# Kernel tuning notes

Measured on AMD Instinct MI355X. Metric: run time of the kernel, lower is better.

Reference implementation:

```python
import jax, jax.numpy as jnp
import numpy as np

NQ = 100000  # Query nodes
NP = 100000  # Product nodes
E = 600000   # edges per relation
D_IN = 128
D_H = 128
# relation r: (src_type, dst_type); 0=Query, 1=Product
# 0: Click Q->P, 1: reverse_Click P->Q, 2: reverse_QueryResult P->Q, 3: QueryResult Q->P
REL = [(0, 1), (1, 0), (1, 0), (0, 1)]
N_NODES = [NQ, NP]


def setup_inputs() -> dict:
    key = jax.random.key(0)
    ks = jax.random.split(key, 12)
    s = 1.0 / np.sqrt(D_IN)  # keep activations well-scaled across 2 layers
    return {
        "x_query": jax.random.normal(ks[0], (NQ, D_IN), jnp.float32),
        "x_product": jax.random.normal(ks[1], (NP, D_IN), jnp.float32),
        "src_idx": jax.random.randint(ks[2], (4, E), 0, NQ, jnp.int32),
        "dst_idx": jax.random.randint(ks[3], (4, E), 0, NP, jnp.int32),
        "W_self1": jax.random.normal(ks[4], (4, D_IN, D_H), jnp.float32) * s,
        "W_neigh1": jax.random.normal(ks[5], (4, D_IN, D_H), jnp.float32) * s,
        "b1": jnp.zeros((4, D_H), jnp.float32),
        "W_self2": jax.random.normal(ks[6], (4, D_H, D_H), jnp.float32) * s,
        "W_neigh2": jax.random.normal(ks[7], (4, D_H, D_H), jnp.float32) * s,
        "b2": jnp.zeros((4, D_H), jnp.float32),
    }


def _hetero_sage_layer(h, W_self, W_neigh, b, src_idx, dst_idx):
    # h: [h_query, h_product]; per-relation SAGEConv(mean), cross-relation sum
    acc = [None, None]
    for r, (s, t) in enumerate(REL):
        nt = N_NODES[t]
        msg = h[s][src_idx[r]]                                   # [E, d] gather
        neigh_sum = jax.ops.segment_sum(msg, dst_idx[r], num_segments=nt)
        deg = jax.ops.segment_sum(jnp.ones((E,), h[s].dtype), dst_idx[r],
                                  num_segments=nt)
        neigh_mean = neigh_sum / jnp.maximum(deg, 1.0)[:, None]
        out = h[t] @ W_self[r] + neigh_mean @ W_neigh[r] + b[r]
        acc[t] = out if acc[t] is None else acc[t] + out
    return acc


def reference(x_query, x_product, src_idx, dst_idx,
              W_self1, W_neigh1, b1, W_self2, W_neigh2, b2):
    h = [x_query, x_product]
    h = _hetero_sage_layer(h, W_self1, W_neigh1, b1, src_idx, dst_idx)
    h = [jax.nn.relu(v) for v in h]  # ReLU only between layers
    h = _hetero_sage_layer(h, W_self2, W_neigh2, b2, src_idx, dst_idx)
    return (h[0], h[1])  # (H_query, H_product)
```

## Files before the change

### kernel.cpp

```cpp
#include <hip/hip_runtime.h>
#include <hip/hip_bf16.h>

#define N_NODES 100000
#define NEDGE   600000
#define SCAN_B  1024
#define NBLK    98
#define BSHIFT  9
#define NBUCK   196
#define BCAP    3456

typedef __attribute__((ext_vector_type(8))) short bf16x8;
typedef __attribute__((ext_vector_type(4))) short s16x4;
typedef __attribute__((ext_vector_type(4))) float f32x4;
typedef __attribute__((ext_vector_type(4))) unsigned u32x4;
typedef __attribute__((ext_vector_type(2))) int int2v;

__device__ __forceinline__ short f2bf(float f) {
  union { float f; unsigned u; } x; x.f = f;
  unsigned r = x.u + 0x7FFFu + ((x.u >> 16) & 1u);
  return (short)(r >> 16);
}

__global__ __launch_bounds__(256) void bin_k(const int* __restrict__ sidx,
                                             const int* __restrict__ didx,
                                             int* __restrict__ bincnt,
                                             int2v* __restrict__ stage) {
  __shared__ int hist[NBUCK];
  __shared__ int base[NBUCK];
  int r = blockIdx.y, t = threadIdx.x;
  int e0 = blockIdx.x * 2048 + t;
  const int* dd = didx + (size_t)r * NEDGE;
  const int* ss = sidx + (size_t)r * NEDGE;
  for (int i = t; i < NBUCK; i += 256) hist[i] = 0;
  __syncthreads();
  int sv[8], dv[8], bu[8], lr[8];
#pragma unroll
  for (int j = 0; j < 8; ++j) {
    int e = e0 + j * 256;
    if (e < NEDGE) {
      dv[j] = dd[e]; sv[j] = ss[e];
      bu[j] = dv[j] >> BSHIFT;
      lr[j] = atomicAdd(&hist[bu[j]], 1);
    }
  }
  __syncthreads();
  for (int i = t; i < NBUCK; i += 256)
    base[i] = atomicAdd(&bincnt[r * NBUCK + i], hist[i]);
  __syncthreads();
#pragma unroll
  for (int j = 0; j < 8; ++j) {
    int e = e0 + j * 256;
    if (e < NEDGE)
      stage[(size_t)(r * NBUCK + bu[j]) * BCAP + base[bu[j]] + lr[j]] =
          (int2v){sv[j], dv[j]};
  }
}

__global__ __launch_bounds__(256) void hist_k(const int2v* __restrict__ stage,
                                              const int* __restrict__ bincnt,
                                              int* __restrict__ cnt) {
  __shared__ int h[512];
  int bu = blockIdx.x, r = blockIdx.y, t = threadIdx.x;
  int len = bincnt[r * NBUCK + bu];
  const int2v* sg = stage + (size_t)(r * NBUCK + bu) * BCAP;
  h[t] = 0; h[t + 256] = 0;
  __syncthreads();
  int lo = bu << BSHIFT;
  for (int i = t; i < len; i += 256) atomicAdd(&h[sg[i].y - lo], 1);
  __syncthreads();
  int d0 = lo + t;
  if (d0 < N_NODES)       cnt[r * N_NODES + d0]       = h[t];
  if (d0 + 256 < N_NODES) cnt[r * N_NODES + d0 + 256] = h[t + 256];
}

__global__ __launch_bounds__(256) void scan1_k(const int* __restrict__ cnt,
                                               int* __restrict__ bsum) {
  __shared__ int lds[256];
  int b = blockIdx.x, r = blockIdx.y, t = threadIdx.x;
  int i0 = b * SCAN_B + t * 4;
  int s = 0;
#pragma unroll
  for (int j = 0; j < 4; ++j)
    if (i0 + j < N_NODES) s += cnt[r * N_NODES + i0 + j];
  lds[t] = s;
  __syncthreads();
  for (int st = 128; st > 0; st >>= 1) {
    if (t < st) lds[t] += lds[t + st];
    __syncthreads();
  }
  if (t == 0) bsum[r * NBLK + b] = lds[0];
}

__global__ __launch_bounds__(128) void scan2_k(int* __restrict__ bsum) {
  __shared__ int buf[128];
  int t = threadIdx.x;
  for (int r = 0; r < 4; ++r) {
    int v = (t < NBLK) ? bsum[r * NBLK + t] : 0;
    buf[t] = v;
    __syncthreads();
    for (int st = 1; st < 128; st <<= 1) {
      int x = (t >= st) ? buf[t - st] : 0;
      __syncthreads();
      buf[t] += x;
      __syncthreads();
    }
    if (t < NBLK) bsum[r * NBLK + t] = buf[t] - v;
    __syncthreads();
  }
}

__global__ __launch_bounds__(256) void scan3_k(const int* __restrict__ cnt,
                                               const int* __restrict__ bsum,
                                               int* __restrict__ off) {
  __shared__ int lds[256];
  int b = blockIdx.x, r = blockIdx.y, t = threadIdx.x;
  int i0 = b * SCAN_B + t * 4;
  int c[4] = {0, 0, 0, 0};
#pragma unroll
  for (int j = 0; j < 4; ++j)
    if (i0 + j < N_NODES) c[j] = cnt[r * N_NODES + i0 + j];
  int s = c[0] + c[1] + c[2] + c[3];
  lds[t] = s;
  __syncthreads();
  for (int st = 1; st < 256; st <<= 1) {
    int x = (t >= st) ? lds[t - st] : 0;
    __syncthreads();
    lds[t] += x;
    __syncthreads();
  }
  int run = bsum[r * NBLK + b] + lds[t] - s;
  int* o = off + r * (N_NODES + 1);
#pragma unroll
  for (int j = 0; j < 4; ++j) {
    if (i0 + j < N_NODES) { o[i0 + j] = run; run += c[j]; }
  }
  if (b == 0 && t == 0) o[N_NODES] = NEDGE;
}

__global__ __launch_bounds__(256) void place_k(const int2v* __restrict__ stage,
                                               const int* __restrict__ bincnt,
                                               const int* __restrict__ off,
                                               int* __restrict__ csr) {
  __shared__ int ofl[512];
  __shared__ int cur[512];
  int bu = blockIdx.x, r = blockIdx.y, t = threadIdx.x;
  int len = bincnt[r * NBUCK + bu];
  const int2v* sg = stage + (size_t)(r * NBUCK + bu) * BCAP;
  const int* of = off + r * (N_NODES + 1);
  int* cs = csr + (size_t)r * NEDGE;
  int lo = bu << BSHIFT;
  int d0 = lo + t;
  ofl[t]       = (d0 < N_NODES) ? of[d0] : 0;
  ofl[t + 256] = (d0 + 256 < N_NODES) ? of[d0 + 256] : 0;
  cur[t] = 0; cur[t + 256] = 0;
  __syncthreads();
  for (int i = t; i < len; i += 256) {
    int2v sd = sg[i];
    int dl = sd.y - lo;
    int pos = ofl[dl] + atomicAdd(&cur[dl], 1);
    cs[pos] = sd.x;
  }
}

__global__ __launch_bounds__(256) void cvt2_k(const float* __restrict__ x0,
                                              const float* __restrict__ x1,
                                              unsigned* __restrict__ o0,
                                              unsigned* __restrict__ o1) {
  const float* x = blockIdx.y ? x1 : x0;
  unsigned* o = blockIdx.y ? o1 : o0;
  int i = blockIdx.x * 256 + threadIdx.x;
  if (i >= N_NODES * 16) return;
  f32x4 v0 = ((const f32x4*)x)[i * 2];
  f32x4 v1 = ((const f32x4*)x)[i * 2 + 1];
  unsigned r0 = (unsigned)(unsigned short)f2bf(v0[0]) |
                ((unsigned)(unsigned short)f2bf(v0[1]) << 16);
  unsigned r1 = (unsigned)(unsigned short)f2bf(v0[2]) |
                ((unsigned)(unsigned short)f2bf(v0[3]) << 16);
  unsigned r2 = (unsigned)(unsigned short)f2bf(v1[0]) |
                ((unsigned)(unsigned short)f2bf(v1[1]) << 16);
  unsigned r3 = (unsigned)(unsigned short)f2bf(v1[2]) |
                ((unsigned)(unsigned short)f2bf(v1[3]) << 16);
  ((u32x4*)o)[i] = (u32x4){r0, r1, r2, r3};
}

__global__ __launch_bounds__(256) void prep_w_k(const float* __restrict__ Ws1,
                                                const float* __restrict__ Wn1,
                                                const float* __restrict__ Ws2,
                                                const float* __restrict__ Wn2,
                                                short* __restrict__ WTp) {
  int tid = blockIdx.x * 256 + threadIdx.x;
  int lane = tid & 63;
  int n0 = (tid >> 6) & 7;
  int idx3 = tid >> 9;
  int k0 = idx3 % 12;
  int lt = idx3 / 12;
  int l = lt >> 1, t = lt & 1;
  const float* Wself  = l ? Ws2 : Ws1;
  const float* Wneigh = l ? Wn2 : Wn1;
  int rA = t ? 0 : 1, rB = t ? 3 : 2;
  int n = n0 * 16 + (lane & 15);
  int kbase = k0 * 32 + (lane >> 4) * 8;
  short out[8];
#pragma unroll
  for (int j = 0; j < 8; ++j) {
    int k = kbase + j;
    int kk = k & 127, blk = k >> 7;
    float v;
    if (blk == 0)      v = Wself[rA * 16384 + kk * 128 + n] + Wself[rB * 16384 + kk * 128 + n];
    else if (blk == 1) v = Wneigh[rA * 16384 + kk * 128 + n];
    else               v = Wneigh[rB * 16384 + kk * 128 + n];
    out[j] = f2bf(v);
  }
  s16x4* dst = (s16x4*)&WTp[tid * 8];
  dst[0] = *(s16x4*)&out[0];
  dst[1] = *(s16x4*)&out[4];
}

__global__ __launch_bounds__(256) void prep_b_k(const float* __restrict__ b1,
                                                const float* __restrict__ b2,
                                                float* __restrict__ biasc) {
  int tid = blockIdx.x * 256 + threadIdx.x;
  if (tid >= 512) return;
  int l = tid >> 8, t = (tid >> 7) & 1, c = tid & 127;
  const float* b = l ? b2 : b1;
  int rA = t ? 0 : 1, rB = t ? 3 : 2;
  biasc[tid] = b[rA * 128 + c] + b[rB * 128 + c];
}

#define ACC8(u, a)                                            \
  {                                                           \
    _Pragma("unroll") for (int q = 0; q < 4; ++q) {           \
      union { unsigned w; float f; } lo_, hi_;                \
      lo_.w = (u)[q] << 16; hi_.w = (u)[q] & 0xffff0000u;     \
      (a)[2 * q] += lo_.f; (a)[2 * q + 1] += hi_.f;           \
    }                                                         \
  }

__device__ __forceinline__ int clampi(int q, int p0, int p1) {
  int t = q < p1 ? q : p0;
  return t < NEDGE ? t : 0;
}

__global__ __launch_bounds__(256) void gather2_k(
    const unsigned* __restrict__ src0, const unsigned* __restrict__ src1,
    const int* __restrict__ csr, const int* __restrict__ off,
    unsigned* __restrict__ m00, unsigned* __restrict__ m01,
    unsigned* __restrict__ m10, unsigned* __restrict__ m11) {
  int wv = __builtin_amdgcn_readfirstlane(threadIdx.x >> 6);
  int wid = blockIdx.x * 4 + wv;
  int lane = threadIdx.x & 63;
  int type = wid >= N_NODES;
  int n = type ? wid - N_NODES : wid;
  const unsigned* src = type ? src1 : src0;
  const int* csrA = csr + (type ? 0 : 1) * NEDGE;
  const int* csrB = csr + (type ? 3 : 2) * NEDGE;
  const int* offA = off + (type ? 0 : 1) * (N_NODES + 1);
  const int* offB = off + (type ? 3 : 2) * (N_NODES + 1);
  unsigned* mA = type ? m10 : m00;
  unsigned* mB = type ? m11 : m01;
  int pA0 = offA[n], pA1 = offA[n + 1];
  int pB0 = offB[n], pB1 = offB[n + 1];
  int degA = pA1 - pA0, degB = pB1 - pB0;
  int rowg = lane >> 4;
  int colg = lane & 15;
  float a[8] = {}, b[8] = {};
  {
    int ia0 = csrA[clampi(pA0 + rowg,     pA0, pA1)];
    int ia1 = csrA[clampi(pA0 + 4 + rowg, pA0, pA1)];
    int ib0 = csrB[clampi(pB0 + rowg,     pB0, pB1)];
    int ib1 = csrB[clampi(pB0 + 4 + rowg, pB0, pB1)];
    u32x4 ua0 = *(const u32x4*)(src + (size_t)ia0 * 64 + colg * 4);
    u32x4 ua1 = *(const u32x4*)(src + (size_t)ia1 * 64 + colg * 4);
    u32x4 ub0 = *(const u32x4*)(src + (size_t)ib0 * 64 + colg * 4);
    u32x4 ub1 = *(const u32x4*)(src + (size_t)ib1 * 64 + colg * 4);
    if (pA0 + rowg     < pA1) ACC8(ua0, a);
    if (pA0 + 4 + rowg < pA1) ACC8(ua1, a);
    if (pB0 + rowg     < pB1) ACC8(ub0, b);
    if (pB0 + 4 + rowg < pB1) ACC8(ub1, b);
  }
  for (int p = pA0 + 8; p < pA1; p += 8) {
    int i0 = csrA[clampi(p + rowg,     pA0, pA1)];
    int i1 = csrA[clampi(p + 4 + rowg, pA0, pA1)];
    u32x4 u0 = *(const u32x4*)(src + (size_t)i0 * 64 + colg * 4);
    u32x4 u1 = *(const u32x4*)(src + (size_t)i1 * 64 + colg * 4);
    if (p + rowg     < pA1) ACC8(u0, a);
    if (p + 4 + rowg < pA1) ACC8(u1, a);
  }
  for (int p = pB0 + 8; p < pB1; p += 8) {
    int i0 = csrB[clampi(p + rowg,     pB0, pB1)];
    int i1 = csrB[clampi(p + 4 + rowg, pB0, pB1)];
    u32x4 u0 = *(const u32x4*)(src + (size_t)i0 * 64 + colg * 4);
    u32x4 u1 = *(const u32x4*)(src + (size_t)i1 * 64 + colg * 4);
    if (p + rowg     < pB1) ACC8(u0, b);
    if (p + 4 + rowg < pB1) ACC8(u1, b);
  }
#pragma unroll
  for (int q = 0; q < 8; ++q) {
    a[q] += __shfl_xor(a[q], 16); a[q] += __shfl_xor(a[q], 32);
    b[q] += __shfl_xor(b[q], 16); b[q] += __shfl_xor(b[q], 32);
  }
  if (rowg == 0) {
    float invA = 1.0f / (float)(degA > 1 ? degA : 1);
    float invB = 1.0f / (float)(degB > 1 ? degB : 1);
    u32x4 wa, wb;
#pragma unroll
    for (int q = 0; q < 4; ++q) {
      wa[q] = (unsigned)(unsigned short)f2bf(a[2 * q] * invA) |
              ((unsigned)(unsigned short)f2bf(a[2 * q + 1] * invA) << 16);
      wb[q] = (unsigned)(unsigned short)f2bf(b[2 * q] * invB) |
              ((unsigned)(unsigned short)f2bf(b[2 * q + 1] * invB) << 16);
    }
    *(u32x4*)(mA + (size_t)n * 64 + colg * 4) = wa;
    *(u32x4*)(mB + (size_t)n * 64 + colg * 4) = wb;
  }
}

template<int OUT_RELU_BF16>
__global__ __launch_bounds__(256) void gemm2_k(
    const short* __restrict__ self0, const short* __restrict__ self1,
    const short* __restrict__ mA0, const short* __restrict__ mB0,
    const short* __restrict__ mA1, const short* __restrict__ mB1,
    const short* __restrict__ WTpL, const float* __restrict__ biascL,
    void* __restrict__ out0, void* __restrict__ out1) {
  __shared__ short Wlds[6 * 8 * 512];
  int type = blockIdx.y;
  const short* selfp = type ? self1 : self0;
  const short* meanA = type ? mA1 : mA0;
  const short* meanB = type ? mB1 : mB0;
  const short* WTp = WTpL + type * 49152;
  const float* biasc = biascL + type * 128;
  void* outp = type ? out1 : out0;
  int tid = threadIdx.x;
  int lane = tid & 63, wave = tid >> 6;
  int rowbase = blockIdx.x * 128 + wave * 32;
  int r0 = rowbase + (lane & 15), r1 = r0 + 16;
  int rc0 = r0 < N_NODES ? r0 : N_NODES - 1;
  int rc1 = r1 < N_NODES ? r1 : N_NODES - 1;
  int kg = lane >> 4;
  f32x4 acc[2][8] = {};
  for (int half = 0; half < 2; ++half) {
    __syncthreads();
    const f32x4* s = (const f32x4*)WTp + half * 3072;
    f32x4* dst = (f32x4*)Wlds;
#pragma unroll
    for (int i = 0; i < 12; ++i) dst[tid + i * 256] = s[tid + i * 256];
    __syncthreads();
    for (int k0h = 0; k0h < 6; ++k0h) {
      int k0 = half * 6 + k0h;
      int kin = (k0 & 3) * 32 + kg * 8;
      const short* mp = (k0 < 4) ? selfp : ((k0 < 8) ? meanA : meanB);
      bf16x8 a0 = *(const bf16x8*)(mp + (size_t)rc0 * 128 + kin);
      bf16x8 a1 = *(const bf16x8*)(mp + (size_t)rc1 * 128 + kin);
      const short* wb = &Wlds[k0h * 4096 + lane * 8];
#pragma unroll
      for (int n0 = 0; n0 < 8; ++n0) {
        bf16x8 b = *(const bf16x8*)(wb + n0 * 512);
        acc[0][n0] = __builtin_amdgcn_mfma_f32_16x16x32_bf16(a0, b, acc[0][n0], 0, 0, 0);
        acc[1][n0] = __builtin_amdgcn_mfma_f32_16x16x32_bf16(a1, b, acc[1][n0], 0, 0, 0);
      }
    }
  }
  int colb = lane & 15, rloc = kg * 4;
#pragma unroll
  for (int mt = 0; mt < 2; ++mt) {
    int rb = rowbase + mt * 16 + rloc;
#pragma unroll
    for (int n0 = 0; n0 < 8; ++n0) {
      int cc = n0 * 16 + colb;
      float bv = biasc[cc];
#pragma unroll
      for (int j = 0; j < 4; ++j) {
        int rr = rb + j;
        if (rr < N_NODES) {
          float v = acc[mt][n0][j] + bv;
          if (OUT_RELU_BF16) {
            ((short*)outp)[(size_t)rr * 128 + cc] = f2bf(v > 0.f ? v : 0.f);
          } else {
            ((float*)outp)[(size_t)rr * 128 + cc] = v;
          }
        }
      }
    }
  }
}

extern "C" void kernel_launch(void* const* d_in, const int* in_sizes, int n_in,
                              void* d_out, int out_size, void* d_ws, size_t ws_size,
                              hipStream_t stream) {
  (void)in_sizes; (void)n_in; (void)out_size; (void)ws_size;
  const float* xq  = (const float*)d_in[0];
  const float* xp  = (const float*)d_in[1];
  const int*   src = (const int*)d_in[2];
  const int*   dst = (const int*)d_in[3];
  const float* Ws1 = (const float*)d_in[4];
  const float* Wn1 = (const float*)d_in[5];
  const float* b1  = (const float*)d_in[6];
  const float* Ws2 = (const float*)d_in[7];
  const float* Wn2 = (const float*)d_in[8];
  const float* b2  = (const float*)d_in[9];

  char* w = (char*)d_ws;
  int*   cnt    = (int*)w;      w += (size_t)4 * N_NODES * 4;
  int*   bincnt = (int*)w;      w += 4096;
  int*   off    = (int*)w;      w += (size_t)4 * (N_NODES + 1) * 4;
  int*   csr    = (int*)w;      w += (size_t)4 * NEDGE * 4;
  short* meanA  = (short*)w;    w += (size_t)N_NODES * 128 * 2;
  short* meanB  = (short*)w;    w += (size_t)N_NODES * 128 * 2;
  short* h1q    = (short*)w;    w += (size_t)N_NODES * 128 * 2;
  short* h1p    = (short*)w;    w += (size_t)N_NODES * 128 * 2;
  short* xqb    = (short*)w;    w += (size_t)N_NODES * 128 * 2;
  short* xpb    = (short*)w;    w += (size_t)N_NODES * 128 * 2;
  short* WTp    = (short*)w;    w += (size_t)4 * 49152 * 2;
  float* biasc  = (float*)w;    w += 512 * 4;
  int*   bsum   = (int*)w;      w += 4 * 128 * 4;
  int2v* stage  = (int2v*)meanA;
  unsigned* mL1C = (unsigned*)d_out;
  unsigned* mL1D = mL1C + (size_t)N_NODES * 64;
  unsigned* mL2C = (unsigned*)xqb;
  unsigned* mL2D = (unsigned*)xpb;

  dim3 b256(256);
  const int bgrid = (NEDGE + 2047) / 2048;
  const int ggrid = (N_NODES + 127) / 128;
  const int wgrid = 2 * N_NODES / 4;
  const int cgrid = (N_NODES * 16 + 255) / 256;

  hipMemsetAsync(bincnt, 0, 4096, stream);
  bin_k<<<dim3(bgrid, 4), b256, 0, stream>>>(src, dst, bincnt, stage);
  hist_k<<<dim3(NBUCK, 4), b256, 0, stream>>>(stage, bincnt, cnt);
  scan1_k<<<dim3(NBLK, 4), b256, 0, stream>>>(cnt, bsum);
  scan2_k<<<dim3(1), dim3(128), 0, stream>>>(bsum);
  scan3_k<<<dim3(NBLK, 4), b256, 0, stream>>>(cnt, bsum, off);
  place_k<<<dim3(NBUCK, 4), b256, 0, stream>>>(stage, bincnt, off, csr);
  prep_w_k<<<dim3(384), b256, 0, stream>>>(Ws1, Wn1, Ws2, Wn2, WTp);
  prep_b_k<<<dim3(2), b256, 0, stream>>>(b1, b2, biasc);
  cvt2_k<<<dim3(cgrid, 2), b256, 0, stream>>>(xq, xp, (unsigned*)xqb, (unsigned*)xpb);

  gather2_k<<<wgrid, b256, 0, stream>>>((const unsigned*)xpb, (const unsigned*)xqb,
      csr, off, (unsigned*)meanA, (unsigned*)meanB, mL1C, mL1D);
  gemm2_k<1><<<dim3(ggrid, 2), b256, 0, stream>>>(
      xqb, xpb, meanA, meanB, (const short*)mL1C, (const short*)mL1D,
      WTp, biasc, h1q, h1p);

  gather2_k<<<wgrid, b256, 0, stream>>>((const unsigned*)h1p, (const unsigned*)h1q,
      csr, off, (unsigned*)meanA, (unsigned*)meanB, mL2C, mL2D);
  gemm2_k<0><<<dim3(ggrid, 2), b256, 0, stream>>>(
      h1q, h1p, meanA, meanB, (const short*)mL2C, (const short*)mL2D,
      WTp + 2 * 49152, biasc + 256,
      (float*)d_out, (float*)d_out + (size_t)N_NODES * 128);
}
```

Baseline: 471.9 us.

## Pack staged edges into 32 bits, read weights from global, use nontemporal stores

The binning stage now packs each edge's source index (17 bits) and local destination offset (9 bits) into one 32-bit word instead of an 8-byte pair. This halves the staging traffic in bin, hist and place. The GEMM kernel drops its LDS weight staging and the barriers around it, reading weight fragments straight from global or L2 memory instead. The mean and final fp32 output writes use nontemporal stores. The risks are redundant weight fetches from each wave and the loss of the cache behaviour that LDS staging provided.

```diff
diff --git a/kernel.cpp b/kernel.cpp
--- a/kernel.cpp
+++ b/kernel.cpp
@@ -13,7 +13,6 @@
 typedef __attribute__((ext_vector_type(4))) short s16x4;
 typedef __attribute__((ext_vector_type(4))) float f32x4;
 typedef __attribute__((ext_vector_type(4))) unsigned u32x4;
-typedef __attribute__((ext_vector_type(2))) int int2v;
 
 __device__ __forceinline__ short f2bf(float f) {
   union { float f; unsigned u; } x; x.f = f;
@@ -24,7 +23,7 @@
 __global__ __launch_bounds__(256) void bin_k(const int* __restrict__ sidx,
                                              const int* __restrict__ didx,
                                              int* __restrict__ bincnt,
-                                             int2v* __restrict__ stage) {
+                                             unsigned* __restrict__ stage) {
   __shared__ int hist[NBUCK];
   __shared__ int base[NBUCK];
   int r = blockIdx.y, t = threadIdx.x;
@@ -33,13 +32,14 @@
   const int* ss = sidx + (size_t)r * NEDGE;
   for (int i = t; i < NBUCK; i += 256) hist[i] = 0;
   __syncthreads();
-  int sv[8], dv[8], bu[8], lr[8];
+  unsigned pv[8]; int bu[8], lr[8];
 #pragma unroll
   for (int j = 0; j < 8; ++j) {
     int e = e0 + j * 256;
     if (e < NEDGE) {
-      dv[j] = dd[e]; sv[j] = ss[e];
-      bu[j] = dv[j] >> BSHIFT;
+      int dv = dd[e];
+      bu[j] = dv >> BSHIFT;
+      pv[j] = (unsigned)ss[e] | ((unsigned)(dv & 511) << 17);
       lr[j] = atomicAdd(&hist[bu[j]], 1);
     }
   }
@@ -51,23 +51,22 @@
   for (int j = 0; j < 8; ++j) {
     int e = e0 + j * 256;
     if (e < NEDGE)
-      stage[(size_t)(r * NBUCK + bu[j]) * BCAP + base[bu[j]] + lr[j]] =
-          (int2v){sv[j], dv[j]};
-  }
-}
-
-__global__ __launch_bounds__(256) void hist_k(const int2v* __restrict__ stage,
+      stage[(size_t)(r * NBUCK + bu[j]) * BCAP + base[bu[j]] + lr[j]] = pv[j];
+  }
+}
+
+__global__ __launch_bounds__(256) void hist_k(const unsigned* __restrict__ stage,
                                               const int* __restrict__ bincnt,
                                               int* __restrict__ cnt) {
   __shared__ int h[512];
   int bu = blockIdx.x, r = blockIdx.y, t = threadIdx.x;
   int len = bincnt[r * NBUCK + bu];
-  const int2v* sg = stage + (size_t)(r * NBUCK + bu) * BCAP;
+  const unsigned* sg = stage + (size_t)(r * NBUCK + bu) * BCAP;
   h[t] = 0; h[t + 256] = 0;
   __syncthreads();
+  for (int i = t; i < len; i += 256) atomicAdd(&h[sg[i] >> 17], 1);
+  __syncthreads();
   int lo = bu << BSHIFT;
-  for (int i = t; i < len; i += 256) atomicAdd(&h[sg[i].y - lo], 1);
-  __syncthreads();
   int d0 = lo + t;
   if (d0 < N_NODES)       cnt[r * N_NODES + d0]       = h[t];
   if (d0 + 256 < N_NODES) cnt[r * N_NODES + d0 + 256] = h[t + 256];
@@ -137,7 +136,7 @@
   if (b == 0 && t == 0) o[N_NODES] = NEDGE;
 }
 
-__global__ __launch_bounds__(256) void place_k(const int2v* __restrict__ stage,
+__global__ __launch_bounds__(256) void place_k(const unsigned* __restrict__ stage,
                                                const int* __restrict__ bincnt,
                                                const int* __restrict__ off,
                                                int* __restrict__ csr) {
@@ -145,7 +144,7 @@
   __shared__ int cur[512];
   int bu = blockIdx.x, r = blockIdx.y, t = threadIdx.x;
   int len = bincnt[r * NBUCK + bu];
-  const int2v* sg = stage + (size_t)(r * NBUCK + bu) * BCAP;
+  const unsigned* sg = stage + (size_t)(r * NBUCK + bu) * BCAP;
   const int* of = off + r * (N_NODES + 1);
   int* cs = csr + (size_t)r * NEDGE;
   int lo = bu << BSHIFT;
@@ -155,10 +154,10 @@
   cur[t] = 0; cur[t + 256] = 0;
   __syncthreads();
   for (int i = t; i < len; i += 256) {
-    int2v sd = sg[i];
-    int dl = sd.y - lo;
+    unsigned v = sg[i];
+    int dl = v >> 17;
     int pos = ofl[dl] + atomicAdd(&cur[dl], 1);
-    cs[pos] = sd.x;
+    cs[pos] = (int)(v & 0x1FFFFu);
   }
 }
 
@@ -310,8 +309,8 @@
       wb[q] = (unsigned)(unsigned short)f2bf(b[2 * q] * invB) |
               ((unsigned)(unsigned short)f2bf(b[2 * q + 1] * invB) << 16);
     }
-    *(u32x4*)(mA + (size_t)n * 64 + colg * 4) = wa;
-    *(u32x4*)(mB + (size_t)n * 64 + colg * 4) = wb;
+    __builtin_nontemporal_store(wa, (u32x4*)(mA + (size_t)n * 64 + colg * 4));
+    __builtin_nontemporal_store(wb, (u32x4*)(mB + (size_t)n * 64 + colg * 4));
   }
 }
 
@@ -322,7 +321,6 @@
     const short* __restrict__ mA1, const short* __restrict__ mB1,
     const short* __restrict__ WTpL, const float* __restrict__ biascL,
     void* __restrict__ out0, void* __restrict__ out1) {
-  __shared__ short Wlds[6 * 8 * 512];
   int type = blockIdx.y;
   const short* selfp = type ? self1 : self0;
   const short* meanA = type ? mA1 : mA0;
@@ -338,26 +336,18 @@
   int rc1 = r1 < N_NODES ? r1 : N_NODES - 1;
   int kg = lane >> 4;
   f32x4 acc[2][8] = {};
-  for (int half = 0; half < 2; ++half) {
-    __syncthreads();
-    const f32x4* s = (const f32x4*)WTp + half * 3072;
-    f32x4* dst = (f32x4*)Wlds;
-#pragma unroll
-    for (int i = 0; i < 12; ++i) dst[tid + i * 256] = s[tid + i * 256];
-    __syncthreads();
-    for (int k0h = 0; k0h < 6; ++k0h) {
-      int k0 = half * 6 + k0h;
-      int kin = (k0 & 3) * 32 + kg * 8;
-      const short* mp = (k0 < 4) ? selfp : ((k0 < 8) ? meanA : meanB);
-      bf16x8 a0 = *(const bf16x8*)(mp + (size_t)rc0 * 128 + kin);
-      bf16x8 a1 = *(const bf16x8*)(mp + (size_t)rc1 * 128 + kin);
-      const short* wb = &Wlds[k0h * 4096 + lane * 8];
-#pragma unroll
-      for (int n0 = 0; n0 < 8; ++n0) {
-        bf16x8 b = *(const bf16x8*)(wb + n0 * 512);
-        acc[0][n0] = __builtin_amdgcn_mfma_f32_16x16x32_bf16(a0, b, acc[0][n0], 0, 0, 0);
-        acc[1][n0] = __builtin_amdgcn_mfma_f32_16x16x32_bf16(a1, b, acc[1][n0], 0, 0, 0);
-      }
+#pragma unroll 3
+  for (int k0 = 0; k0 < 12; ++k0) {
+    int kin = (k0 & 3) * 32 + kg * 8;
+    const short* mp = (k0 < 4) ? selfp : ((k0 < 8) ? meanA : meanB);
+    bf16x8 a0 = *(const bf16x8*)(mp + (size_t)rc0 * 128 + kin);
+    bf16x8 a1 = *(const bf16x8*)(mp + (size_t)rc1 * 128 + kin);
+    const short* wb = WTp + (size_t)k0 * 4096 + lane * 8;
+#pragma unroll
+    for (int n0 = 0; n0 < 8; ++n0) {
+      bf16x8 b = *(const bf16x8*)(wb + n0 * 512);
+      acc[0][n0] = __builtin_amdgcn_mfma_f32_16x16x32_bf16(a0, b, acc[0][n0], 0, 0, 0);
+      acc[1][n0] = __builtin_amdgcn_mfma_f32_16x16x32_bf16(a1, b, acc[1][n0], 0, 0, 0);
     }
   }
   int colb = lane & 15, rloc = kg * 4;
@@ -376,7 +366,7 @@
           if (OUT_RELU_BF16) {
             ((short*)outp)[(size_t)rr * 128 + cc] = f2bf(v > 0.f ? v : 0.f);
           } else {
-            ((float*)outp)[(size_t)rr * 128 + cc] = v;
+            __builtin_nontemporal_store(v, (float*)outp + (size_t)rr * 128 + cc);
           }
         }
       }
@@ -413,7 +403,7 @@
   short* WTp    = (short*)w;    w += (size_t)4 * 49152 * 2;
   float* biasc  = (float*)w;    w += 512 * 4;
   int*   bsum   = (int*)w;      w += 4 * 128 * 4;
-  int2v* stage  = (int2v*)meanA;
+  unsigned* stage = (unsigned*)meanA;
   unsigned* mL1C = (unsigned*)d_out;
   unsigned* mL1D = mL1C + (size_t)N_NODES * 64;
   unsigned* mL2C = (unsigned*)xqb;
```

Result: slower. 514.5 us (+9.0%).
